# Kernel optimization log

Hardware: AMD Instinct MI355X
Metric: run time of the kernel (lower is better)

Reference implementation:

```python
import jax, jax.numpy as jnp
import numpy as np

GROUPS = 32  # min(32, 256//4)
EPS = 1e-5


def setup_inputs() -> dict:
    key = jax.random.key(0)
    ks = jax.random.split(key, 4)
    B, C, H, W = 8, 256, 128, 128
    x = jax.random.normal(ks[0], (B, C, H, W), dtype=jnp.float32)
    gn_w = jnp.ones((C,), dtype=jnp.float32)
    gn_b = jnp.zeros((C,), dtype=jnp.float32)
    qkv_w = jax.random.normal(ks[1], (3 * C, C), dtype=jnp.float32) * (C ** -0.5)
    qkv_b = jnp.zeros((3 * C,), dtype=jnp.float32)
    proj_w = jax.random.normal(ks[2], (C, C), dtype=jnp.float32) * (C ** -0.5)
    proj_b = jnp.zeros((C,), dtype=jnp.float32)
    return {"x": x, "gn_w": gn_w, "gn_b": gn_b, "qkv_w": qkv_w,
            "qkv_b": qkv_b, "proj_w": proj_w, "proj_b": proj_b}


def _group_norm(x, w, b):
    B, C, H, W = x.shape
    xg = x.reshape(B, GROUPS, C // GROUPS, H, W)
    mean = xg.mean(axis=(2, 3, 4), keepdims=True)
    var = xg.var(axis=(2, 3, 4), keepdims=True)
    xg = (xg - mean) * jax.lax.rsqrt(var + EPS)
    x = xg.reshape(B, C, H, W)
    return x * w[None, :, None, None] + b[None, :, None, None]


def reference(x, gn_w, gn_b, qkv_w, qkv_b, proj_w, proj_b):
    B, C, H, W = x.shape
    num_heads = 8
    head_dim = C // num_heads
    scale = head_dim ** -0.5

    h = _group_norm(x, gn_w, gn_b)
    # 1x1 conv == per-pixel matmul over channels
    qkv = jnp.einsum('bchw,oc->bohw', h, qkv_w) + qkv_b[None, :, None, None]
    qkv = qkv.reshape(B, 3, num_heads, head_dim, H * W)
    q, k, v = qkv[:, 0], qkv[:, 1], qkv[:, 2]  # each (B, h, head_dim, HW)
    # Faithful to source: contracts over spatial axis d=HW -> (B,h,hd,hd)
    attn = jnp.einsum('bhid,bhjd->bhij', q, k) * scale
    attn = jax.nn.softmax(attn, axis=-1)
    out = jnp.einsum('bhij,bhjd->bhid', attn, v)  # (B, h, head_dim, HW)
    out = out.reshape(B, C, H, W)
    out = jnp.einsum('bchw,oc->bohw', out, proj_w) + proj_b[None, :, None, None]
    return x + out
```

## Files before the change

kernel.cpp:

```cpp
#include <hip/hip_runtime.h>
#include <stdint.h>

typedef __bf16 bf16;
typedef __attribute__((ext_vector_type(8))) __bf16 bf16x8;
typedef __attribute__((ext_vector_type(4))) float f32x4;

#define S_HW 16384
#define N_C 256

__device__ __forceinline__ f32x4 mfma16(bf16x8 a, bf16x8 b, f32x4 c) {
  return __builtin_amdgcn_mfma_f32_16x16x32_bf16(a, b, c, 0, 0, 0);
}
__device__ __forceinline__ void async_ld16(const bf16* g, bf16* l) {
  __builtin_amdgcn_global_load_lds(
      (const __attribute__((address_space(1))) unsigned int*)g,
      (__attribute__((address_space(3))) unsigned int*)l, 16, 0, 0);
}
__device__ __forceinline__ unsigned short bf2u(bf16 h) {
  union { bf16 h; unsigned short u; } c; c.h = h; return c.u;
}
__device__ __forceinline__ bf16 u2bf(unsigned short u) {
  union { unsigned short u; bf16 h; } c; c.u = u; return c.h;
}

__global__ __launch_bounds__(256) void k_split(
    const float* __restrict__ x, bf16* __restrict__ yhi, bf16* __restrict__ ylo,
    bf16* __restrict__ yt, float* __restrict__ Sx) {
  int b = blockIdx.z, c0 = blockIdx.y * 64, s0 = blockIdx.x * 64;
  __shared__ unsigned T[64][65];
  __shared__ float sxl[256];
  int t = threadIdx.x;
  int cl = t >> 2, sg = t & 3;
  size_t off = (size_t)(b * N_C + c0 + cl) * S_HW + s0 + sg * 16;
  const float* xp = x + off;
  bf16x8 hv[2], lv[2];
  float sum = 0.f;
#pragma unroll
  for (int i2 = 0; i2 < 4; i2++) {
    float4 v = *(const float4*)(xp + i2 * 4);
    float f4[4] = {v.x, v.y, v.z, v.w};
#pragma unroll
    for (int k = 0; k < 4; k++) {
      int i = i2 * 4 + k;
      float fv = f4[k];
      bf16 h = (bf16)fv;
      bf16 l = (bf16)(fv - (float)h);
      hv[i >> 3][i & 7] = h;
      lv[i >> 3][i & 7] = l;
      sum += fv;
      T[sg * 16 + i][cl] = (unsigned)bf2u(h) | ((unsigned)bf2u(l) << 16);
    }
  }
  *(bf16x8*)(yhi + off) = hv[0];
  *(bf16x8*)(yhi + off + 8) = hv[1];
  *(bf16x8*)(ylo + off) = lv[0];
  *(bf16x8*)(ylo + off + 8) = lv[1];
  sxl[t] = sum;
  __syncthreads();
  if (t < 64) {
    float s2 = sxl[t * 4] + sxl[t * 4 + 1] + sxl[t * 4 + 2] + sxl[t * 4 + 3];
    atomicAdd(&Sx[b * N_C + c0 + t], s2);
  }
  int sl = t >> 2, cg = t & 3;
  bf16x8 ho[2], lo2[2];
#pragma unroll
  for (int i = 0; i < 16; i++) {
    unsigned u = T[sl][cg * 16 + i];
    ho[i >> 3][i & 7] = u2bf((unsigned short)(u & 0xffffu));
    lo2[i >> 3][i & 7] = u2bf((unsigned short)(u >> 16));
  }
  size_t tb = (size_t)(b * S_HW + s0 + sl) * 512 + c0 + cg * 16;
  *(bf16x8*)(yt + tb) = ho[0];
  *(bf16x8*)(yt + tb + 8) = ho[1];
  *(bf16x8*)(yt + tb + 256) = lo2[0];
  *(bf16x8*)(yt + tb + 256 + 8) = lo2[1];
}

__global__ __launch_bounds__(256) void k_gram(
    const bf16* __restrict__ yhi, const bf16* __restrict__ ylo,
    float* __restrict__ YG3) {
  constexpr int BK = 32;
  constexpr int NT = 64;
  constexpr int BUF = 128 * BK;
  __shared__ __align__(16) bf16 As[3 * BUF];
  __shared__ __align__(16) bf16 Bs[3 * BUF];
  int kc = blockIdx.x * 2048;
  int m0 = (blockIdx.y >> 2) * 128, n0 = (blockIdx.y & 3) * 128;
  int b = blockIdx.z;
  int tid = threadIdx.x, lane = tid & 63, wave = tid >> 6;
  int wm = (wave >> 1) * 64, wn = (wave & 1) * 64;
  const bf16* Ab = yhi + (size_t)(b * N_C + m0) * S_HW;
  const bf16* Bb = (n0 < 256) ? yhi + (size_t)(b * N_C + n0) * S_HW
                              : ylo + (size_t)(b * N_C + n0 - 256) * S_HW;
  f32x4 acc[4][4] = {};
  int fm = lane & 15, fk = (lane >> 4) * 8;

  auto STAGE = [&](int bi, int t) {
    int kt = kc + t * BK;
#pragma unroll
    for (int i = 0; i < 2; i++) {
      int ch = i * 256 + tid;
      int row = ch >> 2, col = (ch & 3) * 8;
      async_ld16(Ab + (size_t)row * S_HW + kt + col,
                 As + bi * BUF + (i * 256 + wave * 64) * 8);
      async_ld16(Bb + (size_t)row * S_HW + kt + col,
                 Bs + bi * BUF + (i * 256 + wave * 64) * 8);
    }
  };

  STAGE(0, 0);
  STAGE(1, 1);
  STAGE(2, 2);
  int bi = 0;
  for (int t = 0; t < NT - 2; t++) {
    asm volatile("s_waitcnt vmcnt(8)" ::: "memory");
    __builtin_amdgcn_s_barrier();
    const bf16* Ap = As + bi * BUF;
    const bf16* Bp = Bs + bi * BUF;
    bf16x8 af[4], bfr[4];
#pragma unroll
    for (int q = 0; q < 4; q++) {
      af[q] = *(const bf16x8*)(Ap + (wm + q * 16 + fm) * BK + fk);
      bfr[q] = *(const bf16x8*)(Bp + (wn + q * 16 + fm) * BK + fk);
    }
    asm volatile("s_waitcnt lgkmcnt(0)" ::: "memory");
    __builtin_amdgcn_sched_barrier(0);
    __builtin_amdgcn_s_barrier();
    if (t + 3 < NT) STAGE(bi, t + 3);
#pragma unroll
    for (int ti = 0; ti < 4; ti++)
#pragma unroll
      for (int tj = 0; tj < 4; tj++)
        acc[ti][tj] = mfma16(af[ti], bfr[tj], acc[ti][tj]);
    bi = (bi == 2) ? 0 : bi + 1;
  }
#pragma unroll
  for (int pe = 0; pe < 2; pe++) {
    if (pe == 0)
      asm volatile("s_waitcnt vmcnt(4)" ::: "memory");
    else
      asm volatile("s_waitcnt vmcnt(0)" ::: "memory");
    __builtin_amdgcn_s_barrier();
    const bf16* Ap = As + bi * BUF;
    const bf16* Bp = Bs + bi * BUF;
    bf16x8 af[4], bfr[4];
#pragma unroll
    for (int q = 0; q < 4; q++) {
      af[q] = *(const bf16x8*)(Ap + (wm + q * 16 + fm) * BK + fk);
      bfr[q] = *(const bf16x8*)(Bp + (wn + q * 16 + fm) * BK + fk);
    }
#pragma unroll
    for (int ti = 0; ti < 4; ti++)
#pragma unroll
      for (int tj = 0; tj < 4; tj++)
        acc[ti][tj] = mfma16(af[ti], bfr[tj], acc[ti][tj]);
    bi = (bi == 2) ? 0 : bi + 1;
  }
  int quad = lane >> 4, cn = lane & 15;
#pragma unroll
  for (int ti = 0; ti < 4; ti++)
#pragma unroll
    for (int r = 0; r < 4; r++) {
      int m = m0 + wm + ti * 16 + quad * 4 + r;
#pragma unroll
      for (int tj = 0; tj < 4; tj++) {
        int n = n0 + wn + tj * 16 + cn;
        atomicAdd(&YG3[(size_t)(b * N_C + m) * 512 + n], acc[ti][tj][r]);
      }
    }
}

__global__ __launch_bounds__(256) void k_wkt(const float* __restrict__ qkv_w,
                                             float* __restrict__ WkT) {
  int k = blockIdx.x, j = threadIdx.x;
  WkT[k * 256 + j] = qkv_w[(256 + j) * 256 + k];
}

__global__ __launch_bounds__(256) void k_coefs(
    const float* __restrict__ Sx, const float* __restrict__ YG3,
    const float* __restrict__ gn_w, const float* __restrict__ gn_b,
    const float* __restrict__ qkv_w, const float* __restrict__ qkv_b,
    float* __restrict__ a_, float* __restrict__ bv_, float* __restrict__ u_,
    float* __restrict__ vbe) {
  int b = blockIdx.x, t = threadIdx.x;
  __shared__ float sxl[256], gxd[256], gm[32], gr[32], sh[256], bl[256];
  sxl[t] = Sx[b * N_C + t];
  gxd[t] = YG3[(size_t)(b * N_C + t) * 512 + t] +
           2.f * YG3[(size_t)(b * N_C + t) * 512 + 256 + t];
  __syncthreads();
  if (t < 32) {
    float s = 0.f, q2 = 0.f;
#pragma unroll
    for (int i = 0; i < 8; i++) { s += sxl[t * 8 + i]; q2 += gxd[t * 8 + i]; }
    float mean = s * (1.f / 131072.f);
    float var = q2 * (1.f / 131072.f) - mean * mean;
    gm[t] = mean;
    gr[t] = 1.f / sqrtf(var + 1e-5f);
  }
  __syncthreads();
  {
    float A = gn_w[t] * gr[t >> 3];
    float B = gn_b[t] - gm[t >> 3] * A;
    a_[b * N_C + t] = A;
    bv_[b * N_C + t] = B;
    bl[t] = B;
    sh[t] = A * sxl[t] + 16384.f * B;
  }
  __syncthreads();
  for (int r = t; r < 512; r += 256) {
    const float* wp = qkv_w + (size_t)r * 256;
    float acc = 0.f;
    for (int c = 0; c < 256; c++) acc += wp[c] * sh[c];
    u_[b * 512 + r] = acc;
  }
  {
    const float* wp = qkv_w + (size_t)(512 + t) * 256;
    float acc = 0.f;
    for (int c = 0; c < 256; c++) acc += wp[c] * bl[c];
    vbe[b * N_C + t] = acc + qkv_b[512 + t];
  }
}

__global__ __launch_bounds__(256) void k_t1(
    const float* __restrict__ YG3, const float* __restrict__ WkT,
    const float* __restrict__ a_, const float* __restrict__ bv_,
    const float* __restrict__ Sx, float* __restrict__ T1) {
  int tile = blockIdx.x, b = blockIdx.y;
  int i0 = (tile >> 2) * 64, j0 = (tile & 3) * 64;
  __shared__ float As[64][69];
  __shared__ float Bs[64][69];
  __shared__ float al[256], bl[256], sxl[256];
  int t = threadIdx.x;
  al[t] = a_[b * N_C + t];
  bl[t] = bv_[b * N_C + t];
  sxl[t] = Sx[b * N_C + t];
  int cl = t >> 2, qq = (t & 3) * 16;
  int kk = t >> 2, jj = (t & 3) * 16;
  int ti = t >> 4, tj = t & 15;
  float acc[4][4] = {};
  for (int kc = 0; kc < 256; kc += 64) {
    {
      const float* yg = YG3 + (size_t)(b * N_C + i0 + cl) * 512 + kc + qq;
#pragma unroll
      for (int i = 0; i < 16; i++) As[cl][qq + i] = yg[i] + yg[256 + i];
    }
    __syncthreads();
    {
      int cp = kc + kk;
      const float* ygp = YG3 + (size_t)(b * N_C + cp) * 512 + 256 + i0 + jj;
#pragma unroll
      for (int i = 0; i < 16; i++) As[jj + i][kk] += ygp[i];
    }
    __syncthreads();
    {
      int c = i0 + cl;
      float ac = al[c], bc = bl[c], sxc = sxl[c];
#pragma unroll
      for (int i = 0; i < 16; i++) {
        int cp = kc + qq + i;
        As[cl][qq + i] = ac * al[cp] * As[cl][qq + i] + ac * bl[cp] * sxc +
                         bc * al[cp] * sxl[cp] + 16384.f * bc * bl[cp];
      }
    }
    {
      const float* wp = WkT + (size_t)(kc + kk) * 256 + j0 + jj;
#pragma unroll
      for (int i = 0; i < 16; i += 4) {
        float4 v = *(const float4*)(wp + i);
        Bs[kk][jj + i] = v.x; Bs[kk][jj + i + 1] = v.y;
        Bs[kk][jj + i + 2] = v.z; Bs[kk][jj + i + 3] = v.w;
      }
    }
    __syncthreads();
    for (int k = 0; k < 64; k++) {
      float av[4], bv4[4];
#pragma unroll
      for (int ii = 0; ii < 4; ii++) av[ii] = As[ti * 4 + ii][k];
#pragma unroll
      for (int j2 = 0; j2 < 4; j2++) bv4[j2] = Bs[k][tj * 4 + j2];
#pragma unroll
      for (int ii = 0; ii < 4; ii++)
#pragma unroll
        for (int j2 = 0; j2 < 4; j2++) acc[ii][j2] += av[ii] * bv4[j2];
    }
    __syncthreads();
  }
#pragma unroll
  for (int ii = 0; ii < 4; ii++)
#pragma unroll
    for (int j2 = 0; j2 < 4; j2++)
      T1[(size_t)(b * N_C + i0 + ti * 4 + ii) * 256 + j0 + tj * 4 + j2] =
          acc[ii][j2];
}

__global__ __launch_bounds__(256) void k_logits(
    const float* __restrict__ T1, const float* __restrict__ qkv_w,
    const float* __restrict__ qkv_b, const float* __restrict__ u_,
    float* __restrict__ attn) {
  int h = blockIdx.x, b = blockIdx.y;
  __shared__ float Tc[64][33];
  __shared__ float Wql[32][65];
  __shared__ float Ll[32][33];
  __shared__ float uq[32], uk[32], bq[32], bk[32];
  int t = threadIdx.x;
  if (t < 32) {
    uq[t] = u_[b * 512 + h * 32 + t];
    uk[t] = u_[b * 512 + 256 + h * 32 + t];
    bq[t] = qkv_b[h * 32 + t];
    bk[t] = qkv_b[256 + h * 32 + t];
  }
  int i = t & 31, jg = t >> 5;
  float acc[4] = {};
  for (int cc = 0; cc < 256; cc += 64) {
    {
      int c_l = t >> 2, seg = (t & 3) * 8;
      const float* tp = T1 + (size_t)(b * N_C + cc + c_l) * 256 + h * 32 + seg;
      float4 v0 = *(const float4*)tp, v1 = *(const float4*)(tp + 4);
      Tc[c_l][seg] = v0.x; Tc[c_l][seg + 1] = v0.y;
      Tc[c_l][seg + 2] = v0.z; Tc[c_l][seg + 3] = v0.w;
      Tc[c_l][seg + 4] = v1.x; Tc[c_l][seg + 5] = v1.y;
      Tc[c_l][seg + 6] = v1.z; Tc[c_l][seg + 7] = v1.w;
      int row = t >> 3, seg2 = (t & 7) * 8;
      const float* wp = qkv_w + (size_t)(h * 32 + row) * 256 + cc + seg2;
      float4 w0 = *(const float4*)wp, w1 = *(const float4*)(wp + 4);
      Wql[row][seg2] = w0.x; Wql[row][seg2 + 1] = w0.y;
      Wql[row][seg2 + 2] = w0.z; Wql[row][seg2 + 3] = w0.w;
      Wql[row][seg2 + 4] = w1.x; Wql[row][seg2 + 5] = w1.y;
      Wql[row][seg2 + 6] = w1.z; Wql[row][seg2 + 7] = w1.w;
    }
    __syncthreads();
    for (int c = 0; c < 64; c++) {
      float w = Wql[i][c];
#pragma unroll
      for (int j2 = 0; j2 < 4; j2++) acc[j2] += w * Tc[c][jg * 4 + j2];
    }
    __syncthreads();
  }
  const float scale = 0.17677669529663687f;
#pragma unroll
  for (int j2 = 0; j2 < 4; j2++) {
    int j = jg * 4 + j2;
    Ll[i][j] = scale * (acc[j2] + bq[i] * uk[j] + bk[j] * uq[i] +
                        16384.f * bq[i] * bk[j]);
  }
  __syncthreads();
  if (t < 32) {
    float m = -1e30f;
    for (int j = 0; j < 32; j++) m = fmaxf(m, Ll[t][j]);
    float e[32], s = 0.f;
    for (int j = 0; j < 32; j++) { e[j] = expf(Ll[t][j] - m); s += e[j]; }
    float inv = 1.f / s;
    float* ap = attn + (size_t)((b * 8 + h) * 32 + t) * 32;
    for (int j = 0; j < 32; j++) ap[j] = e[j] * inv;
  }
}

__global__ __launch_bounds__(256) void k_m1(const float* __restrict__ proj_w,
                                            const float* __restrict__ attn,
                                            float* __restrict__ M1) {
  int o = blockIdx.x, b = blockIdx.y, t = threadIdx.x;
  __shared__ float at[8192];
  __shared__ float pl[256];
  for (int k = 0; k < 8192; k += 256) at[k + t] = attn[(size_t)b * 8192 + k + t];
  pl[t] = proj_w[(size_t)o * 256 + t];
  __syncthreads();
  int h = t >> 5, j = t & 31;
  float acc = 0.f;
#pragma unroll
  for (int i = 0; i < 32; i++) acc += pl[h * 32 + i] * at[h * 1024 + i * 32 + j];
  M1[(size_t)(b * N_C + o) * 256 + t] = acc;
}

__global__ __launch_bounds__(256) void k_m2(const float* __restrict__ M1,
                                            const float* __restrict__ qkv_w,
                                            float* __restrict__ M2) {
  int tile = blockIdx.x, b = blockIdx.y;
  int i0 = (tile >> 2) * 64, j0 = (tile & 3) * 64;
  __shared__ float As[64][69];
  __shared__ float Bs[64][69];
  int t = threadIdx.x;
  int cl = t >> 2, qq = (t & 3) * 16;
  int kk = t >> 2, jj = (t & 3) * 16;
  int ti = t >> 4, tj = t & 15;
  float acc[4][4] = {};
  for (int kc = 0; kc < 256; kc += 64) {
    {
      const float* mp = M1 + (size_t)(b * N_C + i0 + cl) * 256 + kc + qq;
#pragma unroll
      for (int i = 0; i < 16; i += 4) {
        float4 v = *(const float4*)(mp + i);
        As[cl][qq + i] = v.x; As[cl][qq + i + 1] = v.y;
        As[cl][qq + i + 2] = v.z; As[cl][qq + i + 3] = v.w;
      }
      const float* wp = qkv_w + (size_t)(512 + kc + kk) * 256 + j0 + jj;
#pragma unroll
      for (int i = 0; i < 16; i += 4) {
        float4 v = *(const float4*)(wp + i);
        Bs[kk][jj + i] = v.x; Bs[kk][jj + i + 1] = v.y;
        Bs[kk][jj + i + 2] = v.z; Bs[kk][jj + i + 3] = v.w;
      }
    }
    __syncthreads();
    for (int k = 0; k < 64; k++) {
      float av[4], bv4[4];
#pragma unroll
      for (int ii = 0; ii < 4; ii++) av[ii] = As[ti * 4 + ii][k];
#pragma unroll
      for (int j2 = 0; j2 < 4; j2++) bv4[j2] = Bs[k][tj * 4 + j2];
#pragma unroll
      for (int ii = 0; ii < 4; ii++)
#pragma unroll
        for (int j2 = 0; j2 < 4; j2++) acc[ii][j2] += av[ii] * bv4[j2];
    }
    __syncthreads();
  }
#pragma unroll
  for (int ii = 0; ii < 4; ii++)
#pragma unroll
    for (int j2 = 0; j2 < 4; j2++)
      M2[(size_t)(b * N_C + i0 + ti * 4 + ii) * 256 + j0 + tj * 4 + j2] =
          acc[ii][j2];
}

__global__ __launch_bounds__(256) void k_fa(
    const float* __restrict__ M2, const float* __restrict__ M1,
    const float* __restrict__ a_, const float* __restrict__ vbe,
    const float* __restrict__ proj_b, bf16* __restrict__ FA,
    float* __restrict__ g_) {
  int o = blockIdx.x, b = blockIdx.y, t = threadIdx.x;
  float f = M2[(size_t)(b * N_C + o) * 256 + t] * a_[b * N_C + t] +
            (t == o ? 1.0f : 0.0f);
  bf16 hi = (bf16)f;
  bf16 lo = (bf16)(f - (float)hi);
  FA[(size_t)(b * N_C + o) * 512 + t] = hi;
  FA[(size_t)(b * N_C + o) * 512 + 256 + t] = lo;
  __shared__ float red[256];
  red[t] = M1[(size_t)(b * N_C + o) * 256 + t] * vbe[b * N_C + t];
  __syncthreads();
  for (int s2 = 128; s2 > 0; s2 >>= 1) {
    if (t < s2) red[t] += red[t + s2];
    __syncthreads();
  }
  if (t == 0) g_[b * N_C + o] = red[0] + proj_b[o];
}

__global__ __launch_bounds__(256) void k_final(
    const bf16* __restrict__ FA, const bf16* __restrict__ yt,
    const float* __restrict__ g_, float* __restrict__ out) {
  constexpr int BK = 32;
  constexpr int NT = 24;
  constexpr int BUF = 128 * BK;
  __shared__ __align__(16) bf16 As[3 * BUF];
  __shared__ __align__(16) bf16 Bs[3 * BUF];
  int b = blockIdx.z, m0 = blockIdx.y * 128, n0 = blockIdx.x * 128;
  int tid = threadIdx.x, lane = tid & 63, wave = tid >> 6;
  int wm = (wave >> 1) * 64, wn = (wave & 1) * 64;
  const bf16* Ab = FA + (size_t)(b * N_C + m0) * 512;
  const bf16* Bb = yt + (size_t)(b * S_HW + n0) * 512;
  f32x4 acc[4][4] = {};
  int fm = lane & 15, fk = (lane >> 4) * 8;

  auto STAGE = [&](int bi, int t) {
    int kt = t * BK;
    int ka = (kt < 512) ? kt : kt - 512;
    int kb = (kt < 256) ? kt : kt - 256;
#pragma unroll
    for (int i = 0; i < 2; i++) {
      int ch = i * 256 + tid;
      int row = ch >> 2, col = (ch & 3) * 8;
      async_ld16(Ab + (size_t)row * 512 + ka + col,
                 As + bi * BUF + (i * 256 + wave * 64) * 8);
      async_ld16(Bb + (size_t)row * 512 + kb + col,
                 Bs + bi * BUF + (i * 256 + wave * 64) * 8);
    }
  };

  STAGE(0, 0);
  STAGE(1, 1);
  STAGE(2, 2);
  int bi = 0;
  for (int t = 0; t < NT - 2; t++) {
    asm volatile("s_waitcnt vmcnt(8)" ::: "memory");
    __builtin_amdgcn_s_barrier();
    const bf16* Ap = As + bi * BUF;
    const bf16* Bp = Bs + bi * BUF;
    bf16x8 af[4], bfr[4];
#pragma unroll
    for (int q = 0; q < 4; q++) {
      af[q] = *(const bf16x8*)(Ap + (wm + q * 16 + fm) * BK + fk);
      bfr[q] = *(const bf16x8*)(Bp + (wn + q * 16 + fm) * BK + fk);
    }
    asm volatile("s_waitcnt lgkmcnt(0)" ::: "memory");
    __builtin_amdgcn_sched_barrier(0);
    __builtin_amdgcn_s_barrier();
    if (t + 3 < NT) STAGE(bi, t + 3);
#pragma unroll
    for (int ti = 0; ti < 4; ti++)
#pragma unroll
      for (int tj = 0; tj < 4; tj++)
        acc[ti][tj] = mfma16(af[ti], bfr[tj], acc[ti][tj]);
    bi = (bi == 2) ? 0 : bi + 1;
  }
#pragma unroll
  for (int pe = 0; pe < 2; pe++) {
    if (pe == 0)
      asm volatile("s_waitcnt vmcnt(4)" ::: "memory");
    else
      asm volatile("s_waitcnt vmcnt(0)" ::: "memory");
    __builtin_amdgcn_s_barrier();
    const bf16* Ap = As + bi * BUF;
    const bf16* Bp = Bs + bi * BUF;
    bf16x8 af[4], bfr[4];
#pragma unroll
    for (int q = 0; q < 4; q++) {
      af[q] = *(const bf16x8*)(Ap + (wm + q * 16 + fm) * BK + fk);
      bfr[q] = *(const bf16x8*)(Bp + (wn + q * 16 + fm) * BK + fk);
    }
#pragma unroll
    for (int ti = 0; ti < 4; ti++)
#pragma unroll
      for (int tj = 0; tj < 4; tj++)
        acc[ti][tj] = mfma16(af[ti], bfr[tj], acc[ti][tj]);
    bi = (bi == 2) ? 0 : bi + 1;
  }
  int quad = lane >> 4, cn = lane & 15;
#pragma unroll
  for (int ti = 0; ti < 4; ti++)
#pragma unroll
    for (int r = 0; r < 4; r++) {
      int row = m0 + wm + ti * 16 + quad * 4 + r;
      float gb = g_[b * N_C + row];
#pragma unroll
      for (int tj = 0; tj < 4; tj++) {
        int col = n0 + wn + tj * 16 + cn;
        size_t idx = (size_t)(b * N_C + row) * S_HW + col;
        out[idx] = acc[ti][tj][r] + gb;
      }
    }
}

extern "C" void kernel_launch(void* const* d_in, const int* in_sizes, int n_in,
                              void* d_out, int out_size, void* d_ws,
                              size_t ws_size, hipStream_t stream) {
  const float* x = (const float*)d_in[0];
  const float* gn_w = (const float*)d_in[1];
  const float* gn_b = (const float*)d_in[2];
  const float* qkv_w = (const float*)d_in[3];
  const float* qkv_b = (const float*)d_in[4];
  const float* proj_w = (const float*)d_in[5];
  const float* proj_b = (const float*)d_in[6];
  float* out = (float*)d_out;

  const size_t MB = 1ull << 20;
  char* ws = (char*)d_ws;
  bf16* ylo = (bf16*)ws;
  bf16* yt = (bf16*)(ws + 64 * MB);
  float* YG3 = (float*)(ws + 192 * MB);
  float* M1 = (float*)(ws + 192 * MB);
  bf16* FA = (bf16*)(ws + 194 * MB);
  float* WkT = (float*)(ws + 196 * MB);
  float* attn = (float*)(ws + 196 * MB + 256 * 1024);
  float* Sx = (float*)(ws + 196 * MB + 512 * 1024);
  float* a_ = (float*)(ws + 196 * MB + 520 * 1024);
  float* bv_ = (float*)(ws + 196 * MB + 528 * 1024);
  float* u_ = (float*)(ws + 196 * MB + 536 * 1024);
  float* vbe = (float*)(ws + 196 * MB + 552 * 1024);
  float* g_ = (float*)(ws + 196 * MB + 560 * 1024);
  float* T1 = (float*)(ws + 198 * MB);
  float* M2 = T1;
  bf16* yhi = (bf16*)d_out;

  if (ws_size < 200 * MB) return;

  hipMemsetAsync(YG3, 0, 4 * MB, stream);
  hipMemsetAsync(Sx, 0, 8 * 1024, stream);
  k_split<<<dim3(256, 4, 8), 256, 0, stream>>>(x, yhi, ylo, yt, Sx);
  k_gram<<<dim3(8, 8, 8), 256, 0, stream>>>(yhi, ylo, YG3);
  k_wkt<<<256, 256, 0, stream>>>(qkv_w, WkT);
  k_coefs<<<8, 256, 0, stream>>>(Sx, YG3, gn_w, gn_b, qkv_w, qkv_b, a_, bv_,
                                 u_, vbe);
  k_t1<<<dim3(16, 8), 256, 0, stream>>>(YG3, WkT, a_, bv_, Sx, T1);
  k_logits<<<dim3(8, 8), 256, 0, stream>>>(T1, qkv_w, qkv_b, u_, attn);
  k_m1<<<dim3(256, 8), 256, 0, stream>>>(proj_w, attn, M1);
  k_m2<<<dim3(16, 8), 256, 0, stream>>>(M1, qkv_w, M2);
  k_fa<<<dim3(256, 8), 256, 0, stream>>>(M2, M1, a_, vbe, proj_b, FA, g_);
  k_final<<<dim3(128, 2, 8), 256, 0, stream>>>(FA, yt, g_, out);
}
```

Measured before the change: 539.1 us.

## Fuse M1/M2/FA kernels into one and parallelize coefficient computation

Replaces the three small kernels k_m1, k_m2 and k_fa with one k_pv kernel. It computes the proj_w·attn tile in shared memory, runs the M2 GEMM, and emits the bf16 hi/lo FA split and the g_ bias directly, so the M1 and M2 intermediates never go through global memory. k_coefs is split across 9 blocks per batch so the u_ dot products run in parallel instead of in 8 serial blocks. The two memsets are merged into one. The cost is that each k_pv block recomputes M1 slices redundantly across column tiles.

```diff
diff --git a/kernel.cpp b/kernel.cpp
--- a/kernel.cpp
+++ b/kernel.cpp
@@ -182,8 +182,9 @@
     const float* __restrict__ qkv_w, const float* __restrict__ qkv_b,
     float* __restrict__ a_, float* __restrict__ bv_, float* __restrict__ u_,
     float* __restrict__ vbe) {
-  int b = blockIdx.x, t = threadIdx.x;
+  int b = blockIdx.x, role = blockIdx.y, t = threadIdx.x;
   __shared__ float sxl[256], gxd[256], gm[32], gr[32], sh[256], bl[256];
+  __shared__ float ured[64][4];
   sxl[t] = Sx[b * N_C + t];
   gxd[t] = YG3[(size_t)(b * N_C + t) * 512 + t] +
            2.f * YG3[(size_t)(b * N_C + t) * 512 + 256 + t];
@@ -201,23 +202,30 @@
   {
     float A = gn_w[t] * gr[t >> 3];
     float B = gn_b[t] - gm[t >> 3] * A;
-    a_[b * N_C + t] = A;
-    bv_[b * N_C + t] = B;
     bl[t] = B;
     sh[t] = A * sxl[t] + 16384.f * B;
-  }
-  __syncthreads();
-  for (int r = t; r < 512; r += 256) {
-    const float* wp = qkv_w + (size_t)r * 256;
-    float acc = 0.f;
-    for (int c = 0; c < 256; c++) acc += wp[c] * sh[c];
-    u_[b * 512 + r] = acc;
-  }
-  {
+    if (role == 0) {
+      a_[b * N_C + t] = A;
+      bv_[b * N_C + t] = B;
+    }
+  }
+  __syncthreads();
+  if (role == 0) {
     const float* wp = qkv_w + (size_t)(512 + t) * 256;
     float acc = 0.f;
     for (int c = 0; c < 256; c++) acc += wp[c] * bl[c];
     vbe[b * N_C + t] = acc + qkv_b[512 + t];
+  } else {
+    int r = (role - 1) * 64 + (t >> 2);
+    int seg = (t & 3) * 64;
+    const float* wp = qkv_w + (size_t)r * 256 + seg;
+    float p = 0.f;
+    for (int c = 0; c < 64; c++) p += wp[c] * sh[seg + c];
+    ured[t >> 2][t & 3] = p;
+    __syncthreads();
+    if (t < 64)
+      u_[b * 512 + (role - 1) * 64 + t] =
+          ured[t][0] + ured[t][1] + ured[t][2] + ured[t][3];
   }
 }
 
@@ -355,42 +363,32 @@
   }
 }
 
-__global__ __launch_bounds__(256) void k_m1(const float* __restrict__ proj_w,
-                                            const float* __restrict__ attn,
-                                            float* __restrict__ M1) {
-  int o = blockIdx.x, b = blockIdx.y, t = threadIdx.x;
-  __shared__ float at[8192];
-  __shared__ float pl[256];
-  for (int k = 0; k < 8192; k += 256) at[k + t] = attn[(size_t)b * 8192 + k + t];
-  pl[t] = proj_w[(size_t)o * 256 + t];
-  __syncthreads();
-  int h = t >> 5, j = t & 31;
-  float acc = 0.f;
-#pragma unroll
-  for (int i = 0; i < 32; i++) acc += pl[h * 32 + i] * at[h * 1024 + i * 32 + j];
-  M1[(size_t)(b * N_C + o) * 256 + t] = acc;
-}
-
-__global__ __launch_bounds__(256) void k_m2(const float* __restrict__ M1,
-                                            const float* __restrict__ qkv_w,
-                                            float* __restrict__ M2) {
+__global__ __launch_bounds__(256) void k_pv(
+    const float* __restrict__ proj_w, const float* __restrict__ attn,
+    const float* __restrict__ qkv_w, const float* __restrict__ a_,
+    const float* __restrict__ vbe, const float* __restrict__ proj_b,
+    bf16* __restrict__ FA, float* __restrict__ g_) {
   int tile = blockIdx.x, b = blockIdx.y;
   int i0 = (tile >> 2) * 64, j0 = (tile & 3) * 64;
   __shared__ float As[64][69];
   __shared__ float Bs[64][69];
+  __shared__ float At[2][32][33];
+  __shared__ float gred[64][4];
   int t = threadIdx.x;
   int cl = t >> 2, qq = (t & 3) * 16;
   int kk = t >> 2, jj = (t & 3) * 16;
   int ti = t >> 4, tj = t & 15;
   float acc[4][4] = {};
+  float gacc = 0.f;
   for (int kc = 0; kc < 256; kc += 64) {
-    {
-      const float* mp = M1 + (size_t)(b * N_C + i0 + cl) * 256 + kc + qq;
-#pragma unroll
-      for (int i = 0; i < 16; i += 4) {
-        float4 v = *(const float4*)(mp + i);
-        As[cl][qq + i] = v.x; As[cl][qq + i + 1] = v.y;
-        As[cl][qq + i + 2] = v.z; As[cl][qq + i + 3] = v.w;
+    int h0 = kc >> 5;
+    __syncthreads();
+    {
+      const float* ap = attn + (size_t)b * 8192 + h0 * 1024;
+#pragma unroll
+      for (int i = 0; i < 8; i++) {
+        int idx = t * 8 + i;
+        At[idx >> 10][(idx >> 5) & 31][idx & 31] = ap[idx];
       }
       const float* wp = qkv_w + (size_t)(512 + kc + kk) * 256 + j0 + jj;
 #pragma unroll
@@ -401,6 +399,27 @@
       }
     }
     __syncthreads();
+    {
+      int hl = qq >> 5;
+      int jbase = qq & 31;
+      const float* pp = proj_w + (size_t)(i0 + cl) * 256 + (h0 + hl) * 32;
+      float pr[32];
+#pragma unroll
+      for (int i = 0; i < 32; i += 4) {
+        float4 v = *(const float4*)(pp + i);
+        pr[i] = v.x; pr[i + 1] = v.y; pr[i + 2] = v.z; pr[i + 3] = v.w;
+      }
+#pragma unroll
+      for (int i = 0; i < 16; i++) {
+        int jm = jbase + i;
+        float s = 0.f;
+#pragma unroll
+        for (int ii = 0; ii < 32; ii++) s += pr[ii] * At[hl][ii][jm];
+        As[cl][qq + i] = s;
+        gacc += s * vbe[b * N_C + kc + qq + i];
+      }
+    }
+    __syncthreads();
     for (int k = 0; k < 64; k++) {
       float av[4], bv4[4];
 #pragma unroll
@@ -412,36 +431,31 @@
 #pragma unroll
         for (int j2 = 0; j2 < 4; j2++) acc[ii][j2] += av[ii] * bv4[j2];
     }
-    __syncthreads();
-  }
-#pragma unroll
-  for (int ii = 0; ii < 4; ii++)
-#pragma unroll
-    for (int j2 = 0; j2 < 4; j2++)
-      M2[(size_t)(b * N_C + i0 + ti * 4 + ii) * 256 + j0 + tj * 4 + j2] =
-          acc[ii][j2];
-}
-
-__global__ __launch_bounds__(256) void k_fa(
-    const float* __restrict__ M2, const float* __restrict__ M1,
-    const float* __restrict__ a_, const float* __restrict__ vbe,
-    const float* __restrict__ proj_b, bf16* __restrict__ FA,
-    float* __restrict__ g_) {
-  int o = blockIdx.x, b = blockIdx.y, t = threadIdx.x;
-  float f = M2[(size_t)(b * N_C + o) * 256 + t] * a_[b * N_C + t] +
-            (t == o ? 1.0f : 0.0f);
-  bf16 hi = (bf16)f;
-  bf16 lo = (bf16)(f - (float)hi);
-  FA[(size_t)(b * N_C + o) * 512 + t] = hi;
-  FA[(size_t)(b * N_C + o) * 512 + 256 + t] = lo;
-  __shared__ float red[256];
-  red[t] = M1[(size_t)(b * N_C + o) * 256 + t] * vbe[b * N_C + t];
-  __syncthreads();
-  for (int s2 = 128; s2 > 0; s2 >>= 1) {
-    if (t < s2) red[t] += red[t + s2];
-    __syncthreads();
-  }
-  if (t == 0) g_[b * N_C + o] = red[0] + proj_b[o];
+  }
+  __syncthreads();
+  gred[cl][t & 3] = gacc;
+  __syncthreads();
+  if ((tile & 3) == 0 && t < 64)
+    g_[b * N_C + i0 + t] =
+        gred[t][0] + gred[t][1] + gred[t][2] + gred[t][3] + proj_b[i0 + t];
+  float a4[4];
+  {
+    float4 v = *(const float4*)(a_ + b * N_C + j0 + tj * 4);
+    a4[0] = v.x; a4[1] = v.y; a4[2] = v.z; a4[3] = v.w;
+  }
+#pragma unroll
+  for (int ii = 0; ii < 4; ii++) {
+    int row = i0 + ti * 4 + ii;
+#pragma unroll
+    for (int j2 = 0; j2 < 4; j2++) {
+      int col = j0 + tj * 4 + j2;
+      float f = acc[ii][j2] * a4[j2] + (row == col ? 1.0f : 0.0f);
+      bf16 hi = (bf16)f;
+      bf16 lo = (bf16)(f - (float)hi);
+      FA[(size_t)(b * N_C + row) * 512 + col] = hi;
+      FA[(size_t)(b * N_C + row) * 512 + 256 + col] = lo;
+    }
+  }
 }
 
 __global__ __launch_bounds__(256) void k_final(
@@ -556,7 +570,6 @@
   bf16* ylo = (bf16*)ws;
   bf16* yt = (bf16*)(ws + 64 * MB);
   float* YG3 = (float*)(ws + 192 * MB);
-  float* M1 = (float*)(ws + 192 * MB);
   bf16* FA = (bf16*)(ws + 194 * MB);
   float* WkT = (float*)(ws + 196 * MB);
   float* attn = (float*)(ws + 196 * MB + 256 * 1024);
@@ -567,22 +580,19 @@
   float* vbe = (float*)(ws + 196 * MB + 552 * 1024);
   float* g_ = (float*)(ws + 196 * MB + 560 * 1024);
   float* T1 = (float*)(ws + 198 * MB);
-  float* M2 = T1;
   bf16* yhi = (bf16*)d_out;
 
   if (ws_size < 200 * MB) return;
 
-  hipMemsetAsync(YG3, 0, 4 * MB, stream);
-  hipMemsetAsync(Sx, 0, 8 * 1024, stream);
+  hipMemsetAsync(YG3, 0, 4 * MB + 520 * 1024, stream);
   k_split<<<dim3(256, 4, 8), 256, 0, stream>>>(x, yhi, ylo, yt, Sx);
   k_gram<<<dim3(8, 8, 8), 256, 0, stream>>>(yhi, ylo, YG3);
   k_wkt<<<256, 256, 0, stream>>>(qkv_w, WkT);
-  k_coefs<<<8, 256, 0, stream>>>(Sx, YG3, gn_w, gn_b, qkv_w, qkv_b, a_, bv_,
-                                 u_, vbe);
+  k_coefs<<<dim3(8, 9), 256, 0, stream>>>(Sx, YG3, gn_w, gn_b, qkv_w, qkv_b,
+                                          a_, bv_, u_, vbe);
   k_t1<<<dim3(16, 8), 256, 0, stream>>>(YG3, WkT, a_, bv_, Sx, T1);
   k_logits<<<dim3(8, 8), 256, 0, stream>>>(T1, qkv_w, qkv_b, u_, attn);
-  k_m1<<<dim3(256, 8), 256, 0, stream>>>(proj_w, attn, M1);
-  k_m2<<<dim3(16, 8), 256, 0, stream>>>(M1, qkv_w, M2);
-  k_fa<<<dim3(256, 8), 256, 0, stream>>>(M2, M1, a_, vbe, proj_b, FA, g_);
+  k_pv<<<dim3(16, 8), 256, 0, stream>>>(proj_w, attn, qkv_w, a_, vbe, proj_b,
+                                        FA, g_);
   k_final<<<dim3(128, 2, 8), 256, 0, stream>>>(FA, yt, g_, out);
 }
```

New measurement: 538.8 us. About the same (-0.1%).
